# Kernel optimization log

Hardware: AMD Instinct MI355X
Metric: run time of the kernel (lower is better)

The kernel has to match this reference:

```python
import jax, jax.numpy as jnp
import numpy as np

H = 1024      # hidden_size
NH = 16       # num_attention_heads
HD = H // NH  # attention_head_size = 64
B, S = 2, 2048


def setup_inputs() -> dict:
    key = jax.random.key(0)
    ks = jax.random.split(key, 8)
    scale = 1.0 / np.sqrt(H)
    return {
        "hidden_states": jax.random.normal(ks[0], (B, S, H), dtype=jnp.float32),
        "attention_mask": jnp.zeros((B, 1, 1, S), dtype=jnp.float32),
        "Wq": jax.random.normal(ks[1], (H, H), dtype=jnp.float32) * scale,
        "bq": jax.random.normal(ks[2], (H,), dtype=jnp.float32) * 0.02,
        "Wk": jax.random.normal(ks[3], (H, H), dtype=jnp.float32) * scale,
        "bk": jax.random.normal(ks[4], (H,), dtype=jnp.float32) * 0.02,
        "Wv": jax.random.normal(ks[5], (H, H), dtype=jnp.float32) * scale,
        "bv": jax.random.normal(ks[6], (H,), dtype=jnp.float32) * 0.02,
    }


def _split_heads(x):
    # [B,S,H] -> [B,NH,S,HD]
    b, s, _ = x.shape
    return x.reshape(b, s, NH, HD).transpose(0, 2, 1, 3)


def reference(hidden_states, attention_mask, Wq, bq, Wk, bk, Wv, bv):
    q = _split_heads(hidden_states @ Wq.T + bq)  # [B,NH,S,HD]
    k = _split_heads(hidden_states @ Wk.T + bk)
    v = _split_heads(hidden_states @ Wv.T + bv)
    scores = jnp.einsum("bhqd,bhkd->bhqk", q, k) / np.sqrt(HD).astype(np.float32)
    scores = scores + attention_mask  # additive mask, broadcast over heads/queries
    weights = jax.nn.softmax(scores, axis=-1)  # dropout is identity in eval mode
    ctx = jnp.einsum("bhqk,bhkd->bhqd", weights, v)  # [B,NH,S,HD]
    return ctx.transpose(0, 2, 1, 3).reshape(hidden_states.shape[0], hidden_states.shape[1], H)
```

## Files before the change

kernel.cpp:

```cpp
#include <hip/hip_runtime.h>
#include <hip/hip_bf16.h>
#include <math.h>

#define HSZ   1024
#define NHEAD 16
#define HDIM  64
#define BATCH 2
#define SEQ   2048

#define LOG2E 1.4426950408889634f

typedef __attribute__((ext_vector_type(8))) short short8;
typedef __attribute__((ext_vector_type(4))) short short4_t;
typedef __attribute__((ext_vector_type(4))) float floatx4;

typedef __attribute__((address_space(1))) const unsigned int gu32;
typedef __attribute__((address_space(3))) unsigned int lu32;

__device__ __forceinline__ void g2lds16(const void* g, void* l) {
    __builtin_amdgcn_global_load_lds((gu32*)g, (lu32*)l, 16, 0, 0);
}

__device__ __forceinline__ short f2bf(float f) {
    union { float f; unsigned u; } v; v.f = f;
    unsigned r = (v.u + 0x7FFF + ((v.u >> 16) & 1)) >> 16;
    return (short)r;
}

__device__ __forceinline__ unsigned pk2(float a, float b) {
    __hip_bfloat162 h = __float22bfloat162_rn(make_float2(a, b));
    return *(unsigned*)&h;
}

__device__ __forceinline__ float ex2(float x) {
#if __has_builtin(__builtin_amdgcn_exp2f)
    return __builtin_amdgcn_exp2f(x);
#else
    return exp2f(x);
#endif
}

__global__ __launch_bounds__(256) void convert_kernel(
    const float4* __restrict__ X, const float4* __restrict__ Wq,
    const float4* __restrict__ Wk, const float4* __restrict__ Wv,
    const float4* __restrict__ Mask,
    short4_t* __restrict__ Xb, short4_t* __restrict__ Wb,
    float4* __restrict__ Mw)
{
    int idx = blockIdx.x * 256 + threadIdx.x;
    if (idx >= 1835008) {
        int t = idx - 1835008;
        float4 f = Mask[t];
        float4 o;
        o.x = f.x * LOG2E; o.y = f.y * LOG2E;
        o.z = f.z * LOG2E; o.w = f.w * LOG2E;
        Mw[t] = o;
        return;
    }
    const float4* src; short4_t* dst;
    if (idx < 1048576) { src = X + idx; dst = Xb + idx; }
    else {
        int t = idx - 1048576;
        int sel = t >> 18;
        int wi  = t & 0x3FFFF;
        src = (sel == 0 ? Wq : sel == 1 ? Wk : Wv) + wi;
        dst = Wb + (sel << 18) + wi;
    }
    float4 f = *src;
    short4_t o;
    o.x = f2bf(f.x); o.y = f2bf(f.y); o.z = f2bf(f.z); o.w = f2bf(f.w);
    *dst = o;
}

__global__ __launch_bounds__(256, 3) void qkv_mfma_kernel(
    const short* __restrict__ Xb, const short* __restrict__ Wb,
    const float* __restrict__ bq, const float* __restrict__ bk,
    const float* __restrict__ bv,
    short* __restrict__ qo, short* __restrict__ ko, short* __restrict__ vT)
{
    __shared__ short Sm[128 * 136];
    short* As = Sm;
    short* Bs = Sm + 8192;

    const int tid  = threadIdx.x;
    const int lane = tid & 63;
    const int w    = tid >> 6;
    const int l    = lane & 15, quad = lane >> 4;
    const int gM   = blockIdx.y * 128;
    const int gN   = blockIdx.x * 128;
    const int wm   = (w >> 1) * 64, wn = (w & 1) * 64;
    const int ci   = lane >> 3, pb = lane & 7;

    floatx4 acc[4][4] = {};

    for (int kt = 0; kt < HSZ / 64; ++kt) {
        const int k0 = kt * 64;
        __syncthreads();
        #pragma unroll
        for (int u = 0; u < 4; ++u) {
            int c  = w * 4 + u;
            int r  = c * 8 + ci;
            int lb = pb ^ (r & 7);
            g2lds16(Xb + (size_t)(gM + r) * HSZ + k0 + lb * 8, &As[c * 512]);
            g2lds16(Wb + (size_t)(gN + r) * HSZ + k0 + lb * 8, &Bs[c * 512]);
        }
        __syncthreads();
        #pragma unroll
        for (int kk = 0; kk < 2; ++kk) {
            short8 a[4], b[4];
            #pragma unroll
            for (int i = 0; i < 4; ++i) {
                int m = wm + i * 16 + l;
                a[i] = *(const short8*)&As[m * 64 + (((quad + kk * 4) ^ (m & 7)) << 3)];
                int n = wn + i * 16 + l;
                b[i] = *(const short8*)&Bs[n * 64 + (((quad + kk * 4) ^ (n & 7)) << 3)];
            }
            #pragma unroll
            for (int i = 0; i < 4; ++i)
                #pragma unroll
                for (int j = 0; j < 4; ++j)
                    acc[i][j] = __builtin_amdgcn_mfma_f32_16x16x32_bf16(
                        a[i], b[j], acc[i][j], 0, 0, 0);
        }
    }

    const int mat = gN >> 10;
    const int bb = gM >> 11, ss0 = gM & (SEQ - 1);

    if (mat == 2) {
        __syncthreads();
        #pragma unroll
        for (int j = 0; j < 4; ++j) {
            int fl = wn + j * 16 + l;
            float bv_ = bv[(gN & 1023) + fl];
            #pragma unroll
            for (int i = 0; i < 4; ++i)
                #pragma unroll
                for (int r = 0; r < 4; ++r)
                    Sm[fl * 136 + wm + i * 16 + quad * 4 + r]
                        = f2bf(acc[i][j][r] + bv_);
        }
        __syncthreads();
        #pragma unroll
        for (int it = 0; it < 16; ++it) {
            int f = (tid >> 5) + it * 8;
            int c = (tid & 31) * 4;
            short4_t val = *(const short4_t*)&Sm[f * 136 + c];
            int b = (c >> 2) & 15;
            int cp = (c & ~63) | ((((b & 8) | ((b & 3) << 1) | ((b >> 2) & 1))) << 2);
            int nft = (gN & 1023) + f;
            int head = nft >> 6, d = nft & 63;
            *(short4_t*)&vT[(((size_t)(bb * NHEAD + head)) * HDIM + d) * SEQ
                            + ss0 + cp] = val;
        }
        return;
    }

    const float* bias = (mat == 0) ? bq : bk;
    short* dst        = (mat == 0) ? qo : ko;
    const float qscale = (mat == 0) ? 0.125f * LOG2E : 1.0f;

    __syncthreads();
    #pragma unroll
    for (int j = 0; j < 4; ++j) {
        int fl = wn + j * 16 + l;
        float bb_ = bias[(gN & 1023) + fl];
        #pragma unroll
        for (int i = 0; i < 4; ++i)
            #pragma unroll
            for (int r = 0; r < 4; ++r)
                Sm[(wm + i * 16 + quad * 4 + r) * 136 + fl]
                    = f2bf((acc[i][j][r] + bb_) * qscale);
    }
    __syncthreads();
    #pragma unroll
    for (int it = 0; it < 8; ++it) {
        int row = (tid >> 4) + it * 16;
        int fc  = (tid & 15) * 8;
        short8 val = *(const short8*)&Sm[row * 136 + fc];
        int nft = (gN & 1023) + fc;
        int head = nft >> 6, d = nft & 63;
        *(short8*)&dst[(((size_t)(bb * NHEAD + head)) * SEQ + ss0 + row) * HDIM + d]
            = val;
    }
}

__global__ __launch_bounds__(256, 4) void attn_kernel(
    const short* __restrict__ Qg, const short* __restrict__ Kg,
    const short* __restrict__ VTg, const float* __restrict__ maskw,
    float* __restrict__ out)
{
    __shared__ alignas(16) short Sh[4][4096];
    __shared__ alignas(16) float Ms[2][64];
    __shared__ alignas(16) float Lx[2][2][64];

    const int tid  = threadIdx.x;
    const int lane = tid & 63;
    const int w    = tid >> 6;
    const int l    = lane & 15, quad = lane >> 4;
    const int idx  = blockIdx.x;
    const int bh   = idx & 31;
    const int qt   = idx >> 5;
    const int batch = bh >> 4, head = bh & 15;
    const int qh = w & 1, kh = w >> 1;
    const int ci = lane >> 3, pb = lane & 7;

    const short* Qb = Qg + ((size_t)bh * SEQ + qt * 64) * HDIM;
    const short* Kb = Kg + (size_t)bh * SEQ * HDIM;
    const short* Vb = VTg + (size_t)bh * HDIM * SEQ;
    const float* mrow = maskw + (size_t)batch * SEQ;

    short* Qst = (short*)&Sh[2][0];

    #pragma unroll
    for (int u = 0; u < 2; ++u) {
        int c = w * 2 + u;
        int r = c * 8 + ci;
        int lb = pb ^ (r & 7);
        g2lds16(Qb + (size_t)r * HDIM + lb * 8, &Qst[c * 512]);
        g2lds16(Kb + (size_t)r * HDIM + lb * 8, &Sh[0][c * 512]);
        g2lds16(Vb + (size_t)r * SEQ + lb * 8, &Sh[1][c * 512]);
    }
    if (tid < 16) g2lds16(mrow + tid * 4, &Ms[0][0]);
    __syncthreads();

    short8 aq[2][2];
    #pragma unroll
    for (int n = 0; n < 2; ++n)
        #pragma unroll
        for (int kk = 0; kk < 2; ++kk) {
            int m = qh * 32 + n * 16 + l;
            aq[n][kk] = *(const short8*)&Qst[m * 64
                          + (((quad + kk * 4) ^ (m & 7)) << 3)];
        }
    __syncthreads();

    floatx4 o[2][4] = {};
    float l_i[2] = {0.f, 0.f};

    for (int kt = 0; kt < SEQ / 64; ++kt) {
        const int cur = kt & 1, nxt = cur ^ 1;
        if (kt + 1 < SEQ / 64) {
            const int r0 = (kt + 1) * 64;
            #pragma unroll
            for (int u = 0; u < 2; ++u) {
                int c = w * 2 + u;
                int r = c * 8 + ci;
                int lb = pb ^ (r & 7);
                g2lds16(Kb + (size_t)(r0 + r) * HDIM + lb * 8, &Sh[2 * nxt][c * 512]);
                g2lds16(Vb + (size_t)r * SEQ + r0 + lb * 8, &Sh[2 * nxt + 1][c * 512]);
            }
            if (tid < 16) g2lds16(mrow + r0 + tid * 4, &Ms[nxt][0]);
        }

        float4 mq[2];
        #pragma unroll
        for (int m = 0; m < 2; ++m)
            mq[m] = *(const float4*)&Ms[cur][kh * 32 + m * 16 + quad * 4];

        floatx4 s[2][2];
        #pragma unroll
        for (int m = 0; m < 2; ++m) {
            floatx4 ini = {mq[m].x, mq[m].y, mq[m].z, mq[m].w};
            #pragma unroll
            for (int n = 0; n < 2; ++n) s[m][n] = ini;
        }
        #pragma unroll
        for (int kk = 0; kk < 2; ++kk) {
            short8 ak[2];
            #pragma unroll
            for (int m = 0; m < 2; ++m) {
                int kr = kh * 32 + m * 16 + l;
                ak[m] = *(const short8*)&Sh[2 * cur][kr * 64
                            + (((quad + kk * 4) ^ (kr & 7)) << 3)];
            }
            #pragma unroll
            for (int m = 0; m < 2; ++m)
                #pragma unroll
                for (int n = 0; n < 2; ++n)
                    s[m][n] = __builtin_amdgcn_mfma_f32_16x16x32_bf16(
                        ak[m], aq[n][kk], s[m][n], 0, 0, 0);
        }

        #pragma unroll
        for (int n = 0; n < 2; ++n) {
            float rs = 0.f;
            #pragma unroll
            for (int m = 0; m < 2; ++m) {
                s[m][n][0] = ex2(s[m][n][0]);
                s[m][n][1] = ex2(s[m][n][1]);
                s[m][n][2] = ex2(s[m][n][2]);
                s[m][n][3] = ex2(s[m][n][3]);
                rs += (s[m][n][0] + s[m][n][1]) + (s[m][n][2] + s[m][n][3]);
            }
            l_i[n] += rs;
        }

        short8 ap[2];
        #pragma unroll
        for (int n = 0; n < 2; ++n) {
            union { unsigned u[4]; short8 s8; } pu;
            pu.u[0] = pk2(s[0][n][0], s[0][n][1]);
            pu.u[1] = pk2(s[0][n][2], s[0][n][3]);
            pu.u[2] = pk2(s[1][n][0], s[1][n][1]);
            pu.u[3] = pk2(s[1][n][2], s[1][n][3]);
            ap[n] = pu.s8;
        }

        short8 bvf[4];
        #pragma unroll
        for (int nd = 0; nd < 4; ++nd) {
            int d = nd * 16 + l;
            bvf[nd] = *(const short8*)&Sh[2 * cur + 1][d * 64
                          + (((kh * 4 + quad) ^ (d & 7)) << 3)];
        }
        #pragma unroll
        for (int nq = 0; nq < 2; ++nq)
            #pragma unroll
            for (int nd = 0; nd < 4; ++nd)
                o[nq][nd] = __builtin_amdgcn_mfma_f32_16x16x32_bf16(
                    ap[nq], bvf[nd], o[nq][nd], 0, 0, 0);

        __syncthreads();
    }

    float* reg = (qh == 0) ? (float*)&Sh[0][0] : (float*)&Sh[2][0];
    if (kh == 1) {
        #pragma unroll
        for (int nq = 0; nq < 2; ++nq)
            #pragma unroll
            for (int nd = 0; nd < 4; ++nd)
                *(floatx4*)&reg[((nq * 4 + nd) * 64 + lane) * 4] = o[nq][nd];
        #pragma unroll
        for (int n = 0; n < 2; ++n) Lx[qh][n][lane] = l_i[n];
    }
    __syncthreads();
    if (kh == 0) {
        #pragma unroll
        for (int nq = 0; nq < 2; ++nq)
            #pragma unroll
            for (int nd = 0; nd < 4; ++nd)
                o[nq][nd] += *(const floatx4*)&reg[((nq * 4 + nd) * 64 + lane) * 4];
        #pragma unroll
        for (int n = 0; n < 2; ++n) {
            float t = l_i[n] + Lx[qh][n][lane];
            t += __shfl_xor(t, 16);
            t += __shfl_xor(t, 32);
            l_i[n] = t;
        }
        #pragma unroll
        for (int nq = 0; nq < 2; ++nq) {
            #pragma unroll
            for (int r = 0; r < 4; ++r) {
                float inv = 1.0f / __shfl(l_i[nq], (lane & 48) + quad * 4 + r);
                int qrow = qt * 64 + qh * 32 + nq * 16 + quad * 4 + r;
                #pragma unroll
                for (int nd = 0; nd < 4; ++nd)
                    out[((size_t)batch * SEQ + qrow) * HSZ + head * HDIM + nd * 16 + l]
                        = o[nq][nd][r] * inv;
            }
        }
    }
}

extern "C" void kernel_launch(void* const* d_in, const int* in_sizes, int n_in,
                              void* d_out, int out_size, void* d_ws, size_t ws_size,
                              hipStream_t stream) {
    const float* hs   = (const float*)d_in[0];
    const float* mask = (const float*)d_in[1];
    const float* Wq   = (const float*)d_in[2];
    const float* bq   = (const float*)d_in[3];
    const float* Wk   = (const float*)d_in[4];
    const float* bk   = (const float*)d_in[5];
    const float* Wv   = (const float*)d_in[6];
    const float* bv   = (const float*)d_in[7];
    float* out = (float*)d_out;

    short* Xb = (short*)d_ws;
    short* Wb = Xb + 4194304;
    short* qb = Wb + 3145728;
    short* kb = qb + 4194304;
    short* vT = kb + 4194304;
    float* Mw = (float*)(vT + 4194304);

    convert_kernel<<<7172, 256, 0, stream>>>(
        (const float4*)hs, (const float4*)Wq, (const float4*)Wk, (const float4*)Wv,
        (const float4*)mask, (short4_t*)Xb, (short4_t*)Wb, (float4*)Mw);

    dim3 g2(3 * HSZ / 128, BATCH * SEQ / 128);
    qkv_mfma_kernel<<<g2, 256, 0, stream>>>(Xb, Wb, bq, bk, bv, qb, kb, vT);

    attn_kernel<<<1024, 256, 0, stream>>>(qb, kb, vT, Mw, out);
}
```

Before: 166.1 us.

## Split attention waves along keys only and software-pipeline QK against PV

Each of the four waves now owns all 64 query rows and a 16-key slice of every key tile, rather than splitting queries and keys two ways. The QK^T MFMA for the next tile is issued after the PV MFMAs of the current tile, and prefetch runs two tiles ahead, so the exp/PV work can overlap the next score computation. PV uses 16x16x16 MFMAs with 4-element P fragments, which lets V^T be stored without the old column permutation. The cost is more accumulators per wave (occupancy hint lowered from 4 to 3 blocks) and a longer three-step cross-wave reduction at the end.

```diff
diff --git a/kernel.cpp b/kernel.cpp
--- a/kernel.cpp
+++ b/kernel.cpp
@@ -39,6 +39,12 @@
     return exp2f(x);
 #endif
 }
+
+#if __has_builtin(__builtin_amdgcn_mfma_f32_16x16x16_bf16)
+#define MFMA16(a, b, c) __builtin_amdgcn_mfma_f32_16x16x16_bf16(a, b, c, 0, 0, 0)
+#else
+#define MFMA16(a, b, c) __builtin_amdgcn_mfma_f32_16x16x16bf16_1k(a, b, c, 0, 0, 0)
+#endif
 
 __global__ __launch_bounds__(256) void convert_kernel(
     const float4* __restrict__ X, const float4* __restrict__ Wq,
@@ -146,12 +152,10 @@
             int f = (tid >> 5) + it * 8;
             int c = (tid & 31) * 4;
             short4_t val = *(const short4_t*)&Sm[f * 136 + c];
-            int b = (c >> 2) & 15;
-            int cp = (c & ~63) | ((((b & 8) | ((b & 3) << 1) | ((b >> 2) & 1))) << 2);
             int nft = (gN & 1023) + f;
             int head = nft >> 6, d = nft & 63;
             *(short4_t*)&vT[(((size_t)(bb * NHEAD + head)) * HDIM + d) * SEQ
-                            + ss0 + cp] = val;
+                            + ss0 + c] = val;
         }
         return;
     }
@@ -185,24 +189,23 @@
     }
 }
 
-__global__ __launch_bounds__(256, 4) void attn_kernel(
+__global__ __launch_bounds__(256, 3) void attn_kernel(
     const short* __restrict__ Qg, const short* __restrict__ Kg,
     const short* __restrict__ VTg, const float* __restrict__ maskw,
     float* __restrict__ out)
 {
     __shared__ alignas(16) short Sh[4][4096];
     __shared__ alignas(16) float Ms[2][64];
-    __shared__ alignas(16) float Lx[2][2][64];
+    __shared__ alignas(16) float Lx[4][4][16];
 
     const int tid  = threadIdx.x;
     const int lane = tid & 63;
-    const int w    = tid >> 6;
+    const int kh   = tid >> 6;
     const int l    = lane & 15, quad = lane >> 4;
     const int idx  = blockIdx.x;
     const int bh   = idx & 31;
     const int qt   = idx >> 5;
     const int batch = bh >> 4, head = bh & 15;
-    const int qh = w & 1, kh = w >> 1;
     const int ci = lane >> 3, pb = lane & 7;
 
     const short* Qb = Qg + ((size_t)bh * SEQ + qt * 64) * HDIM;
@@ -214,7 +217,7 @@
 
     #pragma unroll
     for (int u = 0; u < 2; ++u) {
-        int c = w * 2 + u;
+        int c = kh * 2 + u;
         int r = c * 8 + ci;
         int lb = pb ^ (r & 7);
         g2lds16(Qb + (size_t)r * HDIM + lb * 8, &Qst[c * 512]);
@@ -224,136 +227,170 @@
     if (tid < 16) g2lds16(mrow + tid * 4, &Ms[0][0]);
     __syncthreads();
 
-    short8 aq[2][2];
-    #pragma unroll
-    for (int n = 0; n < 2; ++n)
+    short8 aq[4][2];
+    #pragma unroll
+    for (int n = 0; n < 4; ++n)
         #pragma unroll
         for (int kk = 0; kk < 2; ++kk) {
-            int m = qh * 32 + n * 16 + l;
+            int m = n * 16 + l;
             aq[n][kk] = *(const short8*)&Qst[m * 64
                           + (((quad + kk * 4) ^ (m & 7)) << 3)];
         }
     __syncthreads();
 
-    floatx4 o[2][4] = {};
-    float l_i[2] = {0.f, 0.f};
-
-    for (int kt = 0; kt < SEQ / 64; ++kt) {
-        const int cur = kt & 1, nxt = cur ^ 1;
-        if (kt + 1 < SEQ / 64) {
-            const int r0 = (kt + 1) * 64;
-            #pragma unroll
-            for (int u = 0; u < 2; ++u) {
-                int c = w * 2 + u;
-                int r = c * 8 + ci;
-                int lb = pb ^ (r & 7);
-                g2lds16(Kb + (size_t)(r0 + r) * HDIM + lb * 8, &Sh[2 * nxt][c * 512]);
-                g2lds16(Vb + (size_t)r * SEQ + r0 + lb * 8, &Sh[2 * nxt + 1][c * 512]);
+    #pragma unroll
+    for (int u = 0; u < 2; ++u) {
+        int c = kh * 2 + u;
+        int r = c * 8 + ci;
+        int lb = pb ^ (r & 7);
+        g2lds16(Kb + (size_t)(64 + r) * HDIM + lb * 8, &Sh[2][c * 512]);
+        g2lds16(Vb + (size_t)r * SEQ + 64 + lb * 8, &Sh[3][c * 512]);
+    }
+    if (tid < 16) g2lds16(mrow + 64 + tid * 4, &Ms[1][0]);
+
+    const int akoff0 = (kh * 16 + l) * 64 + (((quad + 0) ^ ((kh * 16 + l) & 7)) << 3);
+    const int akoff1 = (kh * 16 + l) * 64 + (((quad + 4) ^ ((kh * 16 + l) & 7)) << 3);
+    const int blog   = kh * 2 + (quad >> 1);
+    const int bhalf  = (quad & 1) * 4;
+
+    short8 ak0 = *(const short8*)&Sh[0][akoff0];
+    short8 ak1 = *(const short8*)&Sh[0][akoff1];
+    short4_t bvf[4];
+    #pragma unroll
+    for (int nd = 0; nd < 4; ++nd) {
+        int d = nd * 16 + l;
+        bvf[nd] = *(const short4_t*)&Sh[1][d * 64 + ((blog ^ (d & 7)) << 3) + bhalf];
+    }
+    floatx4 s[4];
+    {
+        float4 mq = *(const float4*)&Ms[0][kh * 16 + quad * 4];
+        floatx4 ini = {mq.x, mq.y, mq.z, mq.w};
+        #pragma unroll
+        for (int n = 0; n < 4; ++n) s[n] = ini;
+        #pragma unroll
+        for (int n = 0; n < 4; ++n) {
+            s[n] = __builtin_amdgcn_mfma_f32_16x16x32_bf16(ak0, aq[n][0], s[n], 0, 0, 0);
+            s[n] = __builtin_amdgcn_mfma_f32_16x16x32_bf16(ak1, aq[n][1], s[n], 0, 0, 0);
+        }
+    }
+
+    floatx4 o[4][4] = {};
+    float l_i[4] = {0.f, 0.f, 0.f, 0.f};
+
+    for (int t = 0; t < 32; ++t) {
+        short4_t ap[4];
+        #pragma unroll
+        for (int n = 0; n < 4; ++n) {
+            s[n][0] = ex2(s[n][0]);
+            s[n][1] = ex2(s[n][1]);
+            s[n][2] = ex2(s[n][2]);
+            s[n][3] = ex2(s[n][3]);
+            l_i[n] += (s[n][0] + s[n][1]) + (s[n][2] + s[n][3]);
+            union { unsigned u[2]; short4_t s4; } pu;
+            pu.u[0] = pk2(s[n][0], s[n][1]);
+            pu.u[1] = pk2(s[n][2], s[n][3]);
+            ap[n] = pu.s4;
+        }
+        #pragma unroll
+        for (int nq = 0; nq < 4; ++nq)
+            #pragma unroll
+            for (int nd = 0; nd < 4; ++nd)
+                o[nq][nd] = MFMA16(ap[nq], bvf[nd], o[nq][nd]);
+
+        if (t < 31) {
+            __syncthreads();
+            if (t < 30) {
+                const int r0 = (t + 2) * 64;
+                const int bd = t & 1;
+                #pragma unroll
+                for (int u = 0; u < 2; ++u) {
+                    int c = kh * 2 + u;
+                    int r = c * 8 + ci;
+                    int lb = pb ^ (r & 7);
+                    g2lds16(Kb + (size_t)(r0 + r) * HDIM + lb * 8,
+                            &Sh[2 * bd][c * 512]);
+                    g2lds16(Vb + (size_t)r * SEQ + r0 + lb * 8,
+                            &Sh[2 * bd + 1][c * 512]);
+                }
+                if (tid < 16) g2lds16(mrow + r0 + tid * 4, &Ms[t & 1][0]);
             }
-            if (tid < 16) g2lds16(mrow + r0 + tid * 4, &Ms[nxt][0]);
-        }
-
-        float4 mq[2];
-        #pragma unroll
-        for (int m = 0; m < 2; ++m)
-            mq[m] = *(const float4*)&Ms[cur][kh * 32 + m * 16 + quad * 4];
-
-        floatx4 s[2][2];
-        #pragma unroll
-        for (int m = 0; m < 2; ++m) {
-            floatx4 ini = {mq[m].x, mq[m].y, mq[m].z, mq[m].w};
-            #pragma unroll
-            for (int n = 0; n < 2; ++n) s[m][n] = ini;
-        }
-        #pragma unroll
-        for (int kk = 0; kk < 2; ++kk) {
-            short8 ak[2];
-            #pragma unroll
-            for (int m = 0; m < 2; ++m) {
-                int kr = kh * 32 + m * 16 + l;
-                ak[m] = *(const short8*)&Sh[2 * cur][kr * 64
-                            + (((quad + kk * 4) ^ (kr & 7)) << 3)];
+            const int bb = (t + 1) & 1;
+            ak0 = *(const short8*)&Sh[2 * bb][akoff0];
+            ak1 = *(const short8*)&Sh[2 * bb][akoff1];
+            #pragma unroll
+            for (int nd = 0; nd < 4; ++nd) {
+                int d = nd * 16 + l;
+                bvf[nd] = *(const short4_t*)&Sh[2 * bb + 1]
+                              [d * 64 + ((blog ^ (d & 7)) << 3) + bhalf];
             }
-            #pragma unroll
-            for (int m = 0; m < 2; ++m)
-                #pragma unroll
-                for (int n = 0; n < 2; ++n)
-                    s[m][n] = __builtin_amdgcn_mfma_f32_16x16x32_bf16(
-                        ak[m], aq[n][kk], s[m][n], 0, 0, 0);
-        }
-
-        #pragma unroll
-        for (int n = 0; n < 2; ++n) {
-            float rs = 0.f;
-            #pragma unroll
-            for (int m = 0; m < 2; ++m) {
-                s[m][n][0] = ex2(s[m][n][0]);
-                s[m][n][1] = ex2(s[m][n][1]);
-                s[m][n][2] = ex2(s[m][n][2]);
-                s[m][n][3] = ex2(s[m][n][3]);
-                rs += (s[m][n][0] + s[m][n][1]) + (s[m][n][2] + s[m][n][3]);
+            float4 mq = *(const float4*)&Ms[bb][kh * 16 + quad * 4];
+            floatx4 ini = {mq.x, mq.y, mq.z, mq.w};
+            #pragma unroll
+            for (int n = 0; n < 4; ++n) s[n] = ini;
+            #pragma unroll
+            for (int n = 0; n < 4; ++n) {
+                s[n] = __builtin_amdgcn_mfma_f32_16x16x32_bf16(ak0, aq[n][0], s[n], 0, 0, 0);
+                s[n] = __builtin_amdgcn_mfma_f32_16x16x32_bf16(ak1, aq[n][1], s[n], 0, 0, 0);
             }
-            l_i[n] += rs;
-        }
-
-        short8 ap[2];
-        #pragma unroll
-        for (int n = 0; n < 2; ++n) {
-            union { unsigned u[4]; short8 s8; } pu;
-            pu.u[0] = pk2(s[0][n][0], s[0][n][1]);
-            pu.u[1] = pk2(s[0][n][2], s[0][n][3]);
-            pu.u[2] = pk2(s[1][n][0], s[1][n][1]);
-            pu.u[3] = pk2(s[1][n][2], s[1][n][3]);
-            ap[n] = pu.s8;
-        }
-
-        short8 bvf[4];
-        #pragma unroll
-        for (int nd = 0; nd < 4; ++nd) {
-            int d = nd * 16 + l;
-            bvf[nd] = *(const short8*)&Sh[2 * cur + 1][d * 64
-                          + (((kh * 4 + quad) ^ (d & 7)) << 3)];
-        }
-        #pragma unroll
-        for (int nq = 0; nq < 2; ++nq)
+        }
+    }
+
+    #pragma unroll
+    for (int n = 0; n < 4; ++n) {
+        float v = l_i[n];
+        v += __shfl_xor(v, 16);
+        v += __shfl_xor(v, 32);
+        l_i[n] = v;
+    }
+    float* r0buf = (float*)&Sh[0][0];
+    float* r1buf = (float*)&Sh[2][0];
+    __syncthreads();
+    if (kh != 0 && lane < 16) {
+        #pragma unroll
+        for (int n = 0; n < 4; ++n) Lx[kh][n][lane] = l_i[n];
+    }
+    if (kh == 1 || kh == 3) {
+        float* dstb = (kh == 1) ? r0buf : r1buf;
+        #pragma unroll
+        for (int nq = 0; nq < 4; ++nq)
             #pragma unroll
             for (int nd = 0; nd < 4; ++nd)
-                o[nq][nd] = __builtin_amdgcn_mfma_f32_16x16x32_bf16(
-                    ap[nq], bvf[nd], o[nq][nd], 0, 0, 0);
-
-        __syncthreads();
-    }
-
-    float* reg = (qh == 0) ? (float*)&Sh[0][0] : (float*)&Sh[2][0];
-    if (kh == 1) {
-        #pragma unroll
-        for (int nq = 0; nq < 2; ++nq)
+                *(floatx4*)&dstb[((nq * 4 + nd) * 64 + lane) * 4] = o[nq][nd];
+    }
+    __syncthreads();
+    if (kh == 0 || kh == 2) {
+        const float* srcb = (kh == 0) ? r0buf : r1buf;
+        #pragma unroll
+        for (int nq = 0; nq < 4; ++nq)
             #pragma unroll
             for (int nd = 0; nd < 4; ++nd)
-                *(floatx4*)&reg[((nq * 4 + nd) * 64 + lane) * 4] = o[nq][nd];
-        #pragma unroll
-        for (int n = 0; n < 2; ++n) Lx[qh][n][lane] = l_i[n];
+                o[nq][nd] += *(const floatx4*)&srcb[((nq * 4 + nd) * 64 + lane) * 4];
+    }
+    __syncthreads();
+    if (kh == 2) {
+        #pragma unroll
+        for (int nq = 0; nq < 4; ++nq)
+            #pragma unroll
+            for (int nd = 0; nd < 4; ++nd)
+                *(floatx4*)&r0buf[((nq * 4 + nd) * 64 + lane) * 4] = o[nq][nd];
     }
     __syncthreads();
     if (kh == 0) {
         #pragma unroll
-        for (int nq = 0; nq < 2; ++nq)
+        for (int nq = 0; nq < 4; ++nq)
             #pragma unroll
             for (int nd = 0; nd < 4; ++nd)
-                o[nq][nd] += *(const floatx4*)&reg[((nq * 4 + nd) * 64 + lane) * 4];
-        #pragma unroll
-        for (int n = 0; n < 2; ++n) {
-            float t = l_i[n] + Lx[qh][n][lane];
-            t += __shfl_xor(t, 16);
-            t += __shfl_xor(t, 32);
-            l_i[n] = t;
-        }
-        #pragma unroll
-        for (int nq = 0; nq < 2; ++nq) {
+                o[nq][nd] += *(const floatx4*)&r0buf[((nq * 4 + nd) * 64 + lane) * 4];
+        float lf[4];
+        #pragma unroll
+        for (int n = 0; n < 4; ++n)
+            lf[n] = l_i[n] + Lx[1][n][l] + Lx[2][n][l] + Lx[3][n][l];
+        #pragma unroll
+        for (int nq = 0; nq < 4; ++nq) {
             #pragma unroll
             for (int r = 0; r < 4; ++r) {
-                float inv = 1.0f / __shfl(l_i[nq], (lane & 48) + quad * 4 + r);
-                int qrow = qt * 64 + qh * 32 + nq * 16 + quad * 4 + r;
+                float inv = 1.0f / __shfl(lf[nq], (lane & 48) + quad * 4 + r);
+                int qrow = qt * 64 + nq * 16 + quad * 4 + r;
                 #pragma unroll
                 for (int nd = 0; nd < 4; ++nd)
                     out[((size_t)batch * SEQ + qrow) * HSZ + head * HDIM + nd * 16 + l]
```

Measured after the change: 173.6 us. +4.5%, slower.
